# Optimization experiments

Measured on AMD Instinct MI355X. Metric: run time of the kernel, lower is better.

## Reference

```python
import jax, jax.numpy as jnp
import numpy as np

B, S, D = 32, 4096, 64        # batch, n_vec, n_dim
L = 13                        # n_link_all (chord links: 0, 1, 2, 4, ..., 2048)
NW = 13                       # n_W sparse-multiply rounds
HF, HV = 128, 128             # fnet / vnet hidden widths
NC = 2                        # n_class
VOCAB = 512
OFFSETS = [0] + [2 ** k for k in range(L - 1)]  # static python ints


def setup_inputs() -> dict:
    key = jax.random.key(0)
    ks = jax.random.split(key, 8)
    sn = lambda k, shape, sc: (jax.random.normal(k, shape, jnp.float32) * sc)
    return {
        "inputs": jax.random.randint(ks[0], (B, S), 0, VOCAB),
        "emb":  sn(ks[1], (VOCAB, D), 1.0),          # frozen embedding table
        "fW1":  sn(ks[2], (NW, D, HF), 0.1),         # stacked FNet layer-1 weights
        "fb1":  jnp.zeros((NW, HF), jnp.float32),
        "fW2":  sn(ks[3], (NW, HF, L), 0.1),         # stacked FNet layer-2 weights
        "fb2":  jnp.zeros((NW, L), jnp.float32),
        "vW1":  sn(ks[4], (D, HV), 0.1),
        "vb1":  jnp.zeros((HV,), jnp.float32),
        "vW2":  sn(ks[5], (HV, D), 0.1),
        "vb2":  jnp.zeros((D,), jnp.float32),
        "finW": sn(ks[6], (NC, S * D), 0.02),        # torch Linear weight (out, in)
        "finb": jnp.zeros((NC,), jnp.float32),
    }


def _gelu(x):
    return jax.nn.gelu(x, approximate=False)  # torch nn.GELU default (erf)


def reference(inputs, emb, fW1, fb1, fW2, fb2, vW1, vb1, vW2, vb2, finW, finb):
    X = emb[inputs]                                                  # (B,S,D)
    # all NW FNets at once: (NW,B,S,L)
    H = _gelu(jnp.einsum('bsd,kdh->kbsh', X, fW1) + fb1[:, None, None, :])
    Fs = jnp.einsum('kbsh,khl->kbsl', H, fW2) + fb2[:, None, None, :]
    # VNet
    V = _gelu(X @ vW1 + vb1) @ vW2 + vb2                             # (B,S,D)
    # chord sparse multiply rounds with residual:
    # Z[b,i,:] <- sum_l F[b,i,l] * Z[b,(i+off_l) mod S,:]  ;  Z += V
    Z = V
    for k in range(NW):
        Fk = Fs[k]                                                   # (B,S,L)
        Zn = Fk[..., 0][..., None] * Z                               # offset 0
        for l in range(1, L):
            Zn = Zn + Fk[..., l][..., None] * jnp.roll(Z, -OFFSETS[l], axis=1)
        Z = Zn + V
    # NOTE: original source computes logits from V (Z is overwritten); we
    # also return Z so the sparse-multiply loop stays live.
    out = V.reshape(B, S * D) @ finW.T + finb                        # (B,NC)
    return out, Z
```

## Files before the change

kernel.cpp:

```cpp
#include <hip/hip_runtime.h>
#include <hip/hip_bf16.h>
#include <hip/hip_fp16.h>
#include <math.h>

#define S_LEN   4096
#define B_SZ    32
#define D_DIM   64
#define L_LNK   13
#define NW_R    13
#define HF_W    128
#define HV_W    128
#define VOCAB_N 512
#define NC_N    2

#define NT      1024
#define STRIDE  1024
#define NROW    4
#define MIRROR  512
#define BUFN    (S_LEN + MIRROR)

#define ZSCALE     16.0f
#define ZSCALE_INV 0.0625f

typedef float vf4 __attribute__((ext_vector_type(4)));

__device__ __forceinline__ float gelu_erf(float x) {
    return 0.5f * x * (1.0f + erff(x * 0.70710678118654752440f));
}

__device__ __forceinline__ uint2 pack4h(vf4 v) {
    __half2 a = __float22half2_rn(float2{v.x, v.y});
    __half2 b = __float22half2_rn(float2{v.z, v.w});
    uint2 r;
    r.x = *reinterpret_cast<unsigned int*>(&a);
    r.y = *reinterpret_cast<unsigned int*>(&b);
    return r;
}

__device__ __forceinline__ unsigned pk_fma_lo(unsigned c, unsigned z, unsigned a) {
    unsigned d;
    asm("v_pk_fma_f16 %0, %1, %2, %3 op_sel:[0,0,0] op_sel_hi:[0,1,1]"
        : "=v"(d) : "v"(c), "v"(z), "v"(a));
    return d;
}
__device__ __forceinline__ unsigned pk_fma_hi(unsigned c, unsigned z, unsigned a) {
    unsigned d;
    asm("v_pk_fma_f16 %0, %1, %2, %3 op_sel:[1,0,0] op_sel_hi:[1,1,1]"
        : "=v"(d) : "v"(c), "v"(z), "v"(a));
    return d;
}
__device__ __forceinline__ unsigned pk_mul_lo(unsigned c, unsigned z) {
    unsigned d;
    asm("v_pk_mul_f16 %0, %1, %2 op_sel:[0,0] op_sel_hi:[0,1]"
        : "=v"(d) : "v"(c), "v"(z));
    return d;
}
__device__ __forceinline__ unsigned pk_add(unsigned a, unsigned b) {
    unsigned d;
    asm("v_pk_add_f16 %0, %1, %2" : "=v"(d) : "v"(a), "v"(b));
    return d;
}
__device__ __forceinline__ void pk2_lo(uint2& a, unsigned c, uint2 z) {
    a.x = pk_fma_lo(c, z.x, a.x);
    a.y = pk_fma_lo(c, z.y, a.y);
}
__device__ __forceinline__ void pk2_hi(uint2& a, unsigned c, uint2 z) {
    a.x = pk_fma_hi(c, z.x, a.x);
    a.y = pk_fma_hi(c, z.y, a.y);
}

__global__ __launch_bounds__(128)
void tables_kernel(const float* __restrict__ emb,
                   const float* __restrict__ fW1, const float* __restrict__ fb1,
                   const float* __restrict__ fW2, const float* __restrict__ fb2,
                   const float* __restrict__ vW1, const float* __restrict__ vb1,
                   const float* __restrict__ vW2, const float* __restrict__ vb2,
                   __half* __restrict__ F_table, float* __restrict__ V_table) {
    __shared__ float s_emb[D_DIM];
    __shared__ float s_H[HF_W];
    __shared__ float s_red[2][16];
    const int blk = blockIdx.x;
    const int tid = threadIdx.x;

    if (blk < NW_R * VOCAB_N) {
        const int k = blk >> 9;
        const int t = blk & (VOCAB_N - 1);
        if (tid < D_DIM) s_emb[tid] = emb[t * D_DIM + tid];
        __syncthreads();
        float acc = fb1[k * HF_W + tid];
        const float* w = fW1 + (size_t)k * D_DIM * HF_W + tid;
        #pragma unroll 8
        for (int d = 0; d < D_DIM; ++d) acc += s_emb[d] * w[d * HF_W];
        const float hval = gelu_erf(acc);
        const float* w2 = fW2 + ((size_t)k * HF_W + tid) * L_LNK;
        float p[L_LNK];
        #pragma unroll
        for (int l = 0; l < L_LNK; ++l) p[l] = hval * w2[l];
        #pragma unroll
        for (int o = 1; o < 64; o <<= 1) {
            #pragma unroll
            for (int l = 0; l < L_LNK; ++l) p[l] += __shfl_xor(p[l], o, 64);
        }
        if ((tid & 63) == 0) {
            const int wv = tid >> 6;
            #pragma unroll
            for (int l = 0; l < L_LNK; ++l) s_red[wv][l] = p[l];
        }
        __syncthreads();
        if (tid < L_LNK) {
            float o = fb2[k * L_LNK + tid] + s_red[0][tid] + s_red[1][tid];
            F_table[((size_t)(k * VOCAB_N + t)) * 16 + tid] = __float2half_rn(o);
        }
    } else {
        const int t = blk - NW_R * VOCAB_N;
        if (tid < D_DIM) s_emb[tid] = emb[t * D_DIM + tid];
        __syncthreads();
        float acc = vb1[tid];
        const float* w = vW1 + tid;
        #pragma unroll 8
        for (int d = 0; d < D_DIM; ++d) acc += s_emb[d] * w[d * HV_W];
        s_H[tid] = gelu_erf(acc);
        __syncthreads();
        if (tid < D_DIM) {
            float o = vb2[tid];
            const float* w2 = vW2 + tid;
            #pragma unroll 8
            for (int h = 0; h < HV_W; ++h) o += s_H[h] * w2[h * D_DIM];
            V_table[t * D_DIM + tid] = o;
        }
    }
}

__global__ __launch_bounds__(NT, 8)
void chord_kernel(const int* __restrict__ tok,
                  const __half* __restrict__ F_table,
                  const float* __restrict__ V_table,
                  const float* __restrict__ finW,
                  const float* __restrict__ finb,
                  float* __restrict__ out,
                  float* __restrict__ Zout) {
    __shared__ uint2 Zs[2][BUFN];
    __shared__ float slog[16][2];
    const int n  = blockIdx.x;
    const int b  = n & 31;
    const int ds = ((n >> 5) & 7) * 2 + (n >> 8);
    const int t  = threadIdx.x;
    const vf4* V4 = (const vf4*)V_table;

    unsigned tokf[NROW];
    uint2 Vp[NROW], zp[NROW];
    #pragma unroll
    for (int j = 0; j < NROW; ++j) {
        const int r = t + STRIDE * j;
        const int tk = tok[b * S_LEN + r];
        tokf[j] = (unsigned)tk * 32u;
        vf4 v = V4[tk * 16 + ds];
        v.x *= ZSCALE_INV; v.y *= ZSCALE_INV;
        v.z *= ZSCALE_INV; v.w *= ZSCALE_INV;
        uint2 p = pack4h(v);
        Vp[j] = p; zp[j] = p;
        Zs[0][r] = p;
    }
    if (t < MIRROR) Zs[0][S_LEN + t] = zp[0];

    float l0 = 0.0f, l1 = 0.0f;
    {
        const int rb = ds << 8;
        const float4* W0 = (const float4*)finW;
        const float4* W1 = (const float4*)(finW + (size_t)S_LEN * D_DIM);
        const float4* Vt = (const float4*)V_table;
        #pragma unroll
        for (int q = 0; q < 4; ++q) {
            const int i = t + NT * q;
            const int r = rb + (i >> 4);
            const int c4 = i & 15;
            const int tk = tok[b * S_LEN + r];
            float4 v  = Vt[tk * 16 + c4];
            float4 w0 = W0[(size_t)r * 16 + c4];
            float4 w1 = W1[(size_t)r * 16 + c4];
            l0 += v.x * w0.x + v.y * w0.y + v.z * w0.z + v.w * w0.w;
            l1 += v.x * w1.x + v.y * w1.y + v.z * w1.z + v.w * w1.w;
        }
    }
    #pragma unroll
    for (int o = 32; o > 0; o >>= 1) {
        l0 += __shfl_down(l0, o, 64);
        l1 += __shfl_down(l1, o, 64);
    }
    if ((t & 63) == 0) { slog[t >> 6][0] = l0; slog[t >> 6][1] = l1; }
    __syncthreads();
    if (t == 0) {
        float s0 = 0.0f, s1 = 0.0f;
        #pragma unroll
        for (int i = 0; i < 16; ++i) { s0 += slog[i][0]; s1 += slog[i][1]; }
        if (ds == 0) { s0 += finb[0]; s1 += finb[1]; }
        atomicAdd(&out[b * NC_N + 0], s0);
        atomicAdd(&out[b * NC_N + 1], s1);
    }

    int cur = 0;
    uint2 acc[NROW];
    #pragma unroll 1
    for (int k = 0; k < NW_R; ++k) {
        const char* Fk = (const char*)F_table + (size_t)k * (VOCAB_N * 32);
        const uint2* Zc = Zs[cur];
        uint2* Zn = Zs[cur ^ 1];
        const bool wr = (k < NW_R - 1);
        #pragma unroll
        for (int j = 0; j < NROW; ++j) {
            const int r = t + STRIDE * j;
            const char* Fr = Fk + tokf[j];
            uint4 u0 = *(const uint4*)Fr;
            uint4 u1 = *(const uint4*)(Fr + 16);
            uint2 a, a2;
            a.x = pk_fma_lo(u0.x, zp[j].x, Vp[j].x);
            a.y = pk_fma_lo(u0.x, zp[j].y, Vp[j].y);
            {
                uint2 z32 = Zc[r + 32];
                a2.x = pk_mul_lo(u0.w, z32.x);
                a2.y = pk_mul_lo(u0.w, z32.y);
            }
            pk2_hi(a,  u0.x, Zc[r + 1]);
            pk2_lo(a,  u0.y, Zc[r + 2]);
            pk2_hi(a,  u0.y, Zc[r + 4]);
            pk2_lo(a,  u0.z, Zc[r + 8]);
            pk2_hi(a,  u0.z, Zc[r + 16]);
            pk2_hi(a2, u0.w, Zc[r + 64]);
            pk2_lo(a2, u1.x, Zc[r + 128]);
            pk2_hi(a2, u1.x, Zc[r + 256]);
            pk2_lo(a2, u1.y, Zc[r + 512]);
            pk2_hi(a2, u1.y, zp[(j + 1) & 3]);
            pk2_lo(a2, u1.z, zp[(j + 2) & 3]);
            uint2 s;
            s.x = pk_add(a.x, a2.x);
            s.y = pk_add(a.y, a2.y);
            acc[j] = s;
            if (wr) {
                Zn[r] = s;
                if (j == 0 && t < MIRROR) Zn[S_LEN + t] = s;
            }
        }
        if (wr) {
            #pragma unroll
            for (int j = 0; j < NROW; ++j) zp[j] = acc[j];
        }
        __syncthreads();
        cur ^= 1;
    }

    #pragma unroll
    for (int j = 0; j < NROW; ++j) {
        const int r = t + STRIDE * j;
        __half2 h0 = *reinterpret_cast<__half2*>(&acc[j].x);
        __half2 h1 = *reinterpret_cast<__half2*>(&acc[j].y);
        float2 f0 = __half22float2(h0);
        float2 f1 = __half22float2(h1);
        vf4 o;
        o.x = f0.x * ZSCALE; o.y = f0.y * ZSCALE;
        o.z = f1.x * ZSCALE; o.w = f1.y * ZSCALE;
        *(vf4*)(Zout + (((size_t)b * S_LEN + r) << 6) + ds * 4) = o;
    }
}

extern "C" void kernel_launch(void* const* d_in, const int* in_sizes, int n_in,
                              void* d_out, int out_size, void* d_ws, size_t ws_size,
                              hipStream_t stream) {
    const int*   tok  = (const int*)d_in[0];
    const float* emb  = (const float*)d_in[1];
    const float* fW1  = (const float*)d_in[2];
    const float* fb1  = (const float*)d_in[3];
    const float* fW2  = (const float*)d_in[4];
    const float* fb2  = (const float*)d_in[5];
    const float* vW1  = (const float*)d_in[6];
    const float* vb1  = (const float*)d_in[7];
    const float* vW2  = (const float*)d_in[8];
    const float* vb2  = (const float*)d_in[9];
    const float* finW = (const float*)d_in[10];
    const float* finb = (const float*)d_in[11];

    float* out = (float*)d_out;
    float* Z   = out + B_SZ * NC_N;

    float*  V_table = (float*)d_ws;
    __half* F_table = (__half*)(V_table + VOCAB_N * D_DIM);

    tables_kernel<<<NW_R * VOCAB_N + VOCAB_N, 128, 0, stream>>>(
        emb, fW1, fb1, fW2, fb2, vW1, vb1, vW2, vb2, F_table, V_table);
    chord_kernel<<<512, NT, 0, stream>>>(
        tok, F_table, V_table, finW, finb, out, Z);
}
```

Baseline: 184.8 us.

## Assign adjacent row pairs per thread and use 16-byte LDS loads

Changes the row-to-thread mapping so each thread owns two adjacent sequence rows in each half of the sequence, rather than rows strided by 1024. This allows shared-memory reads and writes of the Z buffer to use 128-bit accesses that cover both rows at once, roughly halving the number of LDS instructions. The offset-1 neighbour now comes from a register, and the offset-1024 and offset-2048 terms are taken from LDS or registers according to the new mapping. The mirror region and the wraparound index handling are adjusted to match, which raises the risk of indexing errors.

```diff
diff --git a/kernel.cpp b/kernel.cpp
--- a/kernel.cpp
+++ b/kernel.cpp
@@ -14,7 +14,6 @@
 #define NC_N    2
 
 #define NT      1024
-#define STRIDE  1024
 #define NROW    4
 #define MIRROR  512
 #define BUFN    (S_LEN + MIRROR)
@@ -64,9 +63,15 @@
     a.x = pk_fma_lo(c, z.x, a.x);
     a.y = pk_fma_lo(c, z.y, a.y);
 }
-__device__ __forceinline__ void pk2_hi(uint2& a, unsigned c, uint2 z) {
-    a.x = pk_fma_hi(c, z.x, a.x);
-    a.y = pk_fma_hi(c, z.y, a.y);
+__device__ __forceinline__ void pkp_lo(uint2& aa, uint2& ab,
+                                       unsigned ca, unsigned cb, uint4 z) {
+    aa.x = pk_fma_lo(ca, z.x, aa.x); aa.y = pk_fma_lo(ca, z.y, aa.y);
+    ab.x = pk_fma_lo(cb, z.z, ab.x); ab.y = pk_fma_lo(cb, z.w, ab.y);
+}
+__device__ __forceinline__ void pkp_hi(uint2& aa, uint2& ab,
+                                       unsigned ca, unsigned cb, uint4 z) {
+    aa.x = pk_fma_hi(ca, z.x, aa.x); aa.y = pk_fma_hi(ca, z.y, aa.y);
+    ab.x = pk_fma_hi(cb, z.z, ab.x); ab.y = pk_fma_hi(cb, z.w, ab.y);
 }
 
 __global__ __launch_bounds__(128)
@@ -139,7 +144,7 @@
                   const float* __restrict__ finb,
                   float* __restrict__ out,
                   float* __restrict__ Zout) {
-    __shared__ uint2 Zs[2][BUFN];
+    __shared__ __align__(16) uint2 Zs[2][BUFN];
     __shared__ float slog[16][2];
     const int n  = blockIdx.x;
     const int b  = n & 31;
@@ -151,7 +156,7 @@
     uint2 Vp[NROW], zp[NROW];
     #pragma unroll
     for (int j = 0; j < NROW; ++j) {
-        const int r = t + STRIDE * j;
+        const int r = (j >> 1) * 2048 + 2 * t + (j & 1);
         const int tk = tok[b * S_LEN + r];
         tokf[j] = (unsigned)tk * 32u;
         vf4 v = V4[tk * 16 + ds];
@@ -161,7 +166,10 @@
         Vp[j] = p; zp[j] = p;
         Zs[0][r] = p;
     }
-    if (t < MIRROR) Zs[0][S_LEN + t] = zp[0];
+    if (t < 256) {
+        Zs[0][S_LEN + 2 * t]     = zp[0];
+        Zs[0][S_LEN + 2 * t + 1] = zp[1];
+    }
 
     float l0 = 0.0f, l1 = 0.0f;
     {
@@ -207,37 +215,50 @@
         uint2* Zn = Zs[cur ^ 1];
         const bool wr = (k < NW_R - 1);
         #pragma unroll
-        for (int j = 0; j < NROW; ++j) {
-            const int r = t + STRIDE * j;
-            const char* Fr = Fk + tokf[j];
-            uint4 u0 = *(const uint4*)Fr;
-            uint4 u1 = *(const uint4*)(Fr + 16);
-            uint2 a, a2;
-            a.x = pk_fma_lo(u0.x, zp[j].x, Vp[j].x);
-            a.y = pk_fma_lo(u0.x, zp[j].y, Vp[j].y);
+        for (int p = 0; p < 2; ++p) {
+            const int j0 = 2 * p, j1 = 2 * p + 1;
+            const int r = (p ? 2048 : 0) + 2 * t;
+            const char* Fr0 = Fk + tokf[j0];
+            const char* Fr1 = Fk + tokf[j1];
+            uint4 u0a = *(const uint4*)Fr0, u1a = *(const uint4*)(Fr0 + 16);
+            uint4 u0b = *(const uint4*)Fr1, u1b = *(const uint4*)(Fr1 + 16);
+            uint2 Aa, Ab, Ba, Bb;
+            Aa.x = pk_fma_lo(u0a.x, zp[j0].x, Vp[j0].x);
+            Aa.y = pk_fma_lo(u0a.x, zp[j0].y, Vp[j0].y);
+            Ab.x = pk_fma_lo(u0b.x, zp[j1].x, Vp[j1].x);
+            Ab.y = pk_fma_lo(u0b.x, zp[j1].y, Vp[j1].y);
             {
-                uint2 z32 = Zc[r + 32];
-                a2.x = pk_mul_lo(u0.w, z32.x);
-                a2.y = pk_mul_lo(u0.w, z32.y);
+                uint4 z32 = *(const uint4*)&Zc[r + 32];
+                Ba.x = pk_mul_lo(u0a.w, z32.x); Ba.y = pk_mul_lo(u0a.w, z32.y);
+                Bb.x = pk_mul_lo(u0b.w, z32.z); Bb.y = pk_mul_lo(u0b.w, z32.w);
             }
-            pk2_hi(a,  u0.x, Zc[r + 1]);
-            pk2_lo(a,  u0.y, Zc[r + 2]);
-            pk2_hi(a,  u0.y, Zc[r + 4]);
-            pk2_lo(a,  u0.z, Zc[r + 8]);
-            pk2_hi(a,  u0.z, Zc[r + 16]);
-            pk2_hi(a2, u0.w, Zc[r + 64]);
-            pk2_lo(a2, u1.x, Zc[r + 128]);
-            pk2_hi(a2, u1.x, Zc[r + 256]);
-            pk2_lo(a2, u1.y, Zc[r + 512]);
-            pk2_hi(a2, u1.y, zp[(j + 1) & 3]);
-            pk2_lo(a2, u1.z, zp[(j + 2) & 3]);
-            uint2 s;
-            s.x = pk_add(a.x, a2.x);
-            s.y = pk_add(a.y, a2.y);
-            acc[j] = s;
+            uint4 z2 = *(const uint4*)&Zc[r + 2];
+            Aa.x = pk_fma_hi(u0a.x, zp[j1].x, Aa.x);
+            Aa.y = pk_fma_hi(u0a.x, zp[j1].y, Aa.y);
+            Ab.x = pk_fma_hi(u0b.x, z2.x, Ab.x);
+            Ab.y = pk_fma_hi(u0b.x, z2.y, Ab.y);
+            pkp_lo(Aa, Ab, u0a.y, u0b.y, z2);
+            pkp_hi(Aa, Ab, u0a.y, u0b.y, *(const uint4*)&Zc[r + 4]);
+            pkp_lo(Aa, Ab, u0a.z, u0b.z, *(const uint4*)&Zc[r + 8]);
+            pkp_hi(Aa, Ab, u0a.z, u0b.z, *(const uint4*)&Zc[r + 16]);
+            pkp_hi(Ba, Bb, u0a.w, u0b.w, *(const uint4*)&Zc[r + 64]);
+            pkp_lo(Ba, Bb, u1a.x, u1b.x, *(const uint4*)&Zc[r + 128]);
+            pkp_hi(Ba, Bb, u1a.x, u1b.x, *(const uint4*)&Zc[r + 256]);
+            pkp_lo(Ba, Bb, u1a.y, u1b.y, *(const uint4*)&Zc[r + 512]);
+            {
+                const int q = p ? ((r + 1024) & (S_LEN - 1)) : (r + 1024);
+                pkp_hi(Ba, Bb, u1a.y, u1b.y, *(const uint4*)&Zc[q]);
+            }
+            pk2_lo(Ba, u1a.z, zp[j0 ^ 2]);
+            pk2_lo(Bb, u1b.z, zp[j1 ^ 2]);
+            uint2 sa, sb;
+            sa.x = pk_add(Aa.x, Ba.x); sa.y = pk_add(Aa.y, Ba.y);
+            sb.x = pk_add(Ab.x, Bb.x); sb.y = pk_add(Ab.y, Bb.y);
+            acc[j0] = sa; acc[j1] = sb;
             if (wr) {
-                Zn[r] = s;
-                if (j == 0 && t < MIRROR) Zn[S_LEN + t] = s;
+                uint4 w4; w4.x = sa.x; w4.y = sa.y; w4.z = sb.x; w4.w = sb.y;
+                *(uint4*)&Zn[r] = w4;
+                if (p == 0 && t < 256) *(uint4*)&Zn[S_LEN + 2 * t] = w4;
             }
         }
         if (wr) {
@@ -250,7 +271,7 @@
 
     #pragma unroll
     for (int j = 0; j < NROW; ++j) {
-        const int r = t + STRIDE * j;
+        const int r = (j >> 1) * 2048 + 2 * t + (j & 1);
         __half2 h0 = *reinterpret_cast<__half2*>(&acc[j].x);
         __half2 h1 = *reinterpret_cast<__half2*>(&acc[j].y);
         float2 f0 = __half22float2(h0);
```

Measured after the change: 196.2 us. +6.1%, slower.
